# Optimization experiments

Measured on AMD Instinct MI355X. Metric: run time of the kernel, lower is better.

Reference implementation:

```python
import jax, jax.numpy as jnp
import numpy as np

V, E, H, O = 50000, 300, 1024, 5
B, T = 64, 512


def setup_inputs() -> dict:
    key = jax.random.key(0)
    ks = jax.random.split(key, 8)
    s_ih = 1.0 / np.sqrt(H)
    return {
        "x": jax.random.randint(ks[0], (B, T), 0, V, dtype=jnp.int32),
        "embeddings": jax.random.normal(ks[1], (V, E), dtype=jnp.float32),
        "W_ih": jax.random.uniform(ks[2], (3 * H, E), jnp.float32, -s_ih, s_ih),
        "W_hh": jax.random.uniform(ks[3], (3 * H, H), jnp.float32, -s_ih, s_ih),
        "b_ih": jax.random.uniform(ks[4], (3 * H,), jnp.float32, -s_ih, s_ih),
        "b_hh": jax.random.uniform(ks[5], (3 * H,), jnp.float32, -s_ih, s_ih),
        "W_fc": jax.random.uniform(ks[6], (O, H), jnp.float32, -s_ih, s_ih),
        "b_fc": jax.random.uniform(ks[7], (O,), jnp.float32, -s_ih, s_ih),
    }


def _gru_last_hidden(emb, W_ih, W_hh, b_ih, b_hh):
    # emb: [B, T, E] -> last hidden state [B, H]
    Hd = W_hh.shape[1]
    # Precompute input contributions for all timesteps: [B, T, 3H]
    gx_all = jnp.einsum("bte,ge->btg", emb, W_ih) + b_ih
    gx_all = jnp.swapaxes(gx_all, 0, 1)  # [T, B, 3H] for scan

    def step(h, gx):
        gh = h @ W_hh.T + b_hh  # [B, 3H]
        xr, xz, xn = jnp.split(gx, 3, axis=-1)
        hr, hz, hn = jnp.split(gh, 3, axis=-1)
        r = jax.nn.sigmoid(xr + hr)
        z = jax.nn.sigmoid(xz + hz)
        n = jnp.tanh(xn + r * hn)
        h_new = (1.0 - z) * n + z * h
        return h_new, None

    h0 = jnp.zeros((emb.shape[0], Hd), dtype=emb.dtype)
    h_last, _ = jax.lax.scan(step, h0, gx_all)
    return h_last


def reference(x, embeddings, W_ih, W_hh, b_ih, b_hh, W_fc, b_fc):
    emb = embeddings[x]  # [B, T, E] embedding lookup (frozen table)
    h_last = _gru_last_hidden(emb, W_ih, W_hh, b_ih, b_hh)  # [B, H]
    return h_last @ W_fc.T + b_fc  # [B, O]
```

## Files before the change

### kernel.cpp

```cpp
#include <hip/hip_runtime.h>
#include <hip/hip_bf16.h>

typedef unsigned short u16;
typedef unsigned int u32;
typedef unsigned long long u64;
typedef __attribute__((ext_vector_type(8))) short bf16x8;
typedef __attribute__((ext_vector_type(4))) float f32x4;
typedef __attribute__((ext_vector_type(4))) unsigned int u32x4;

#define MFMA16(a, b, c) __builtin_amdgcn_mfma_f32_16x16x32_bf16((a), (b), (c), 0, 0, 0)

static constexpr int Ee = 300, EP = 320, Hh = 1024, G3 = 3072;
static constexpr int Bb = 64, Tt = 512;

static constexpr long OFF_GX   = 0L;
static constexpr long OFF_EMB  = 201326592L;
static constexpr long OFF_WIH  = 222298112L;
static constexpr long OFF_WHH  = 224264192L;
static constexpr long OFF_HBUF = 230555648L;

__device__ __forceinline__ u16 f2bf(float f) {
    union { float f; unsigned u; } v; v.f = f;
    unsigned u = v.u;
    return (u16)((u + 0x7fffu + ((u >> 16) & 1u)) >> 16);
}
__device__ __forceinline__ float bf2f(u16 u) {
    union { unsigned u; float f; } v; v.u = ((unsigned)u) << 16;
    return v.f;
}
__device__ __forceinline__ float fast_sigmoid(float x) {
    return 1.f / (1.f + __expf(-x));
}
__device__ __forceinline__ float fast_tanh(float x) {
    float ax = fabsf(x);
    float e = __expf(-2.f * ax);
    float t = (1.f - e) / (1.f + e);
    return copysignf(t, x);
}

static constexpr long R0 = (long)Bb * Tt * EP;
static constexpr long R1 = (long)G3 * EP;
static constexpr long R2 = (long)G3 * Hh;
static constexpr long R3 = 131072;
static constexpr long R5 = 320;

__global__ void prep_kernel(const int* __restrict__ x, const float* __restrict__ emb,
                            const float* __restrict__ wih, const float* __restrict__ whh,
                            const float* __restrict__ bfc,
                            u16* __restrict__ emb_bf, u16* __restrict__ wih_bf,
                            u16* __restrict__ whh_bf, u32* __restrict__ h32,
                            float* __restrict__ out) {
    const long total = R0 + R1 + R2 + R3 + R5;
    for (long i = (long)blockIdx.x * blockDim.x + threadIdx.x; i < total;
         i += (long)gridDim.x * blockDim.x) {
        if (i < R0) {
            const int m = (int)(i / EP), k = (int)(i % EP);
            const int b = m & 63, t = m >> 6;
            u16 v = 0;
            if (k < Ee) {
                const int xi = x[b * Tt + t];
                v = f2bf(emb[(size_t)xi * Ee + k]);
            }
            emb_bf[i] = v;
        } else if (i < R0 + R1) {
            const long j = i - R0;
            const int k = (int)(j % EP);
            const int n = (int)(j / EP);
            wih_bf[j] = (k < Ee) ? f2bf(wih[(size_t)n * Ee + k]) : (u16)0;
        } else if (i < R0 + R1 + R2) {
            const long j = i - R0 - R1;
            whh_bf[j] = f2bf(whh[j]);
        } else if (i < R0 + R1 + R2 + R3) {
            const long j = i - R0 - R1 - R2;
            h32[j] = ((j >> 14) & 1) ? 0xFFFFu : 0u;
        } else {
            const long j = i - R0 - R1 - R2 - R3;
            out[j] = bfc[j % 5];
        }
    }
}

__global__ __launch_bounds__(256, 2)
void gx_gemm(const u16* __restrict__ A, const u16* __restrict__ Bm,
             const float* __restrict__ bih, u16* __restrict__ gx) {
    __shared__ __align__(16) u16 lA[128 * 32];
    __shared__ __align__(16) u16 lB[128 * 32];
    const int tid = threadIdx.x;
    const int lane = tid & 63;
    const int wv = tid >> 6;
    const int quad = lane >> 4, l15 = lane & 15;
    const int m0 = blockIdx.x * 128;
    const int n0 = blockIdx.y * 128;
    const int mo = (wv & 1) * 64, no = (wv >> 1) * 64;
    const int srow = tid >> 2;
    const int sseg = tid & 3;

    f32x4 acc[4][4] = {};

    for (int s = 0; s < 10; ++s) {
        const int k0 = s * 32;
        __syncthreads();
#pragma unroll
        for (int p = 0; p < 2; ++p) {
            const u16* ga = A + (size_t)(m0 + p * 64 + srow) * EP + k0 + sseg * 8;
            u16* la = &lA[p * 2048 + wv * 512];
            __builtin_amdgcn_global_load_lds(
                (const __attribute__((address_space(1))) void*)ga,
                (__attribute__((address_space(3))) void*)la, 16, 0, 0);
            const u16* gb = Bm + (size_t)(n0 + p * 64 + srow) * EP + k0 + sseg * 8;
            u16* lb = &lB[p * 2048 + wv * 512];
            __builtin_amdgcn_global_load_lds(
                (const __attribute__((address_space(1))) void*)gb,
                (__attribute__((address_space(3))) void*)lb, 16, 0, 0);
        }
        __syncthreads();

        bf16x8 af[4], bfr[4];
#pragma unroll
        for (int mt = 0; mt < 4; ++mt)
            af[mt] = *(const bf16x8*)&lA[(mo + mt * 16 + l15) * 32 + quad * 8];
#pragma unroll
        for (int nt = 0; nt < 4; ++nt)
            bfr[nt] = *(const bf16x8*)&lB[(no + nt * 16 + l15) * 32 + quad * 8];
#pragma unroll
        for (int mt = 0; mt < 4; ++mt)
#pragma unroll
            for (int nt = 0; nt < 4; ++nt)
                acc[mt][nt] = MFMA16(af[mt], bfr[nt], acc[mt][nt]);
    }

#pragma unroll
    for (int mt = 0; mt < 4; ++mt) {
        const int mg = m0 + mo + mt * 16 + quad * 4;
        const int t = mg >> 6, b0 = mg & 63;
#pragma unroll
        for (int nt = 0; nt < 4; ++nt) {
            const int n = n0 + no + nt * 16 + l15;
            const float bi = bih[n];
            ushort4 vv;
            vv.x = f2bf(acc[mt][nt][0] + bi);
            vv.y = f2bf(acc[mt][nt][1] + bi);
            vv.z = f2bf(acc[mt][nt][2] + bi);
            vv.w = f2bf(acc[mt][nt][3] + bi);
            *(ushort4*)&gx[((size_t)t * G3 + n) * 64 + b0] = vv;
        }
    }
}

__global__ __launch_bounds__(512, 2)
void scan_kernel(const u16* __restrict__ whh, const float* __restrict__ bhh,
                 const u16* __restrict__ gx, u32* __restrict__ hball,
                 const float* __restrict__ wfc, float* __restrict__ out) {
    __shared__ __align__(16) u16 lh[16 * 1032];
    __shared__ __align__(16) float red[2][3][4][16 * 20];

    const int bid = blockIdx.x;
    const int bg = bid >> 5;
    const int cg = bid & 31;
    const int tid = threadIdx.x;
    const int w = tid >> 6;
    const int lane = tid & 63;
    const int kq = w & 3;
    const int nh = w >> 2;
    const int quad = lane >> 4, l15 = lane & 15;
    const int c0 = cg * 32;
    const bool isGate = (w == 3) || (w == 4);
    const int gnh = (w == 3) ? 0 : 1;

    bf16x8 wf[3][8];
#pragma unroll
    for (int g = 0; g < 3; ++g) {
        const size_t rbase = (size_t)(g * 1024 + c0 + nh * 16 + l15) * 1024;
#pragma unroll
        for (int s = 0; s < 8; ++s)
            wf[g][s] = *(const bf16x8*)&whh[rbase + (kq * 8 + s) * 32 + quad * 8];
    }

    float bh[3][4];
    u16 gxv[3][4];
    float hO[4] = {0.f, 0.f, 0.f, 0.f};
    if (isGate) {
#pragma unroll
        for (int g = 0; g < 3; ++g)
#pragma unroll
            for (int jj = 0; jj < 4; ++jj) {
                const int jglob = c0 + gnh * 16 + quad * 4 + jj;
                bh[g][jj] = bhh[g * 1024 + jglob];
                gxv[g][jj] = gx[((size_t)g * 1024 + jglob) * 64 + bg * 16 + l15];
            }
    }

    u32* hb = hball + (size_t)bg * 32768;
    u64* lhq = (u64*)lh;
    const int t4 = tid << 2;
    const int srow0 = tid >> 8;
    const int sc4 = tid & 255;

    for (int t = 0; t < 512; ++t) {
        const u32* hs = hb + ((t & 1) << 14);
        const u32 tg = (u32)t;

        const u32* p0 = hs + t4;
        const u32* p1 = hs + 2048 + t4;
        const u32* p2 = hs + 4096 + t4;
        const u32* p3 = hs + 6144 + t4;
        const u32* p4 = hs + 8192 + t4;
        const u32* p5 = hs + 10240 + t4;
        const u32* p6 = hs + 12288 + t4;
        const u32* p7 = hs + 14336 + t4;
        u32x4 q0, q1, q2, q3, q4, q5, q6, q7;
        {
            u32 pend = 0xffu;
            do {
                if (pend & 0x01u) asm volatile("global_load_dwordx4 %0, %1, off sc0 sc1" : "=&v"(q0) : "v"(p0) : "memory");
                if (pend & 0x02u) asm volatile("global_load_dwordx4 %0, %1, off sc0 sc1" : "=&v"(q1) : "v"(p1) : "memory");
                if (pend & 0x04u) asm volatile("global_load_dwordx4 %0, %1, off sc0 sc1" : "=&v"(q2) : "v"(p2) : "memory");
                if (pend & 0x08u) asm volatile("global_load_dwordx4 %0, %1, off sc0 sc1" : "=&v"(q3) : "v"(p3) : "memory");
                if (pend & 0x10u) asm volatile("global_load_dwordx4 %0, %1, off sc0 sc1" : "=&v"(q4) : "v"(p4) : "memory");
                if (pend & 0x20u) asm volatile("global_load_dwordx4 %0, %1, off sc0 sc1" : "=&v"(q5) : "v"(p5) : "memory");
                if (pend & 0x40u) asm volatile("global_load_dwordx4 %0, %1, off sc0 sc1" : "=&v"(q6) : "v"(p6) : "memory");
                if (pend & 0x80u) asm volatile("global_load_dwordx4 %0, %1, off sc0 sc1" : "=&v"(q7) : "v"(p7) : "memory");
                asm volatile("s_waitcnt vmcnt(0)" ::: "memory");
                __builtin_amdgcn_sched_barrier(0);
                const u32 before = pend;
#define CHK(bit, qq)                                                          \
                if (pend & (bit)) {                                           \
                    const u32 d = ((qq.x ^ tg) | (qq.y ^ tg) |                \
                                   (qq.z ^ tg) | (qq.w ^ tg)) & 0xffffu;      \
                    if (__all(d == 0)) pend &= ~(u32)(bit);                   \
                }
                CHK(0x01u, q0) CHK(0x02u, q1) CHK(0x04u, q2) CHK(0x08u, q3)
                CHK(0x10u, q4) CHK(0x20u, q5) CHK(0x40u, q6) CHK(0x80u, q7)
#undef CHK
                if (pend && pend == before) __builtin_amdgcn_s_sleep(1);
            } while (pend);
        }

#define UNPK(rr, qq)                                                          \
        {                                                                     \
            const int row = (rr) * 2 + srow0;                                 \
            const u32 lo = (qq.x >> 16) | (qq.y & 0xffff0000u);               \
            const u32 hi = (qq.z >> 16) | (qq.w & 0xffff0000u);               \
            lhq[row * 258 + sc4] = (u64)lo | ((u64)hi << 32);                 \
        }
        UNPK(0, q0) UNPK(1, q1) UNPK(2, q2) UNPK(3, q3)
        UNPK(4, q4) UNPK(5, q5) UNPK(6, q6) UNPK(7, q7)
#undef UNPK
        __syncthreads();

        bf16x8 af[8];
#pragma unroll
        for (int s = 0; s < 8; ++s)
            af[s] = *(const bf16x8*)&lh[l15 * 1032 + kq * 256 + s * 32 + quad * 8];
        f32x4 acc[3] = {};
#pragma unroll
        for (int s = 0; s < 8; ++s) {
            acc[0] = MFMA16(af[s], wf[0][s], acc[0]);
            acc[1] = MFMA16(af[s], wf[1][s], acc[1]);
            acc[2] = MFMA16(af[s], wf[2][s], acc[2]);
        }
#pragma unroll
        for (int g = 0; g < 3; ++g)
#pragma unroll
            for (int r = 0; r < 4; ++r)
                red[nh][g][kq][(quad * 4 + r) * 20 + l15] = acc[g][r];
        __syncthreads();

        if (isGate) {
            f32x4 rr[3][4];
#pragma unroll
            for (int g = 0; g < 3; ++g)
#pragma unroll
                for (int k = 0; k < 4; ++k)
                    rr[g][k] = *(const f32x4*)&red[gnh][g][k][l15 * 20 + quad * 4];
            u32 wtag[4];
#pragma unroll
            for (int jj = 0; jj < 4; ++jj) {
                const float s0 = rr[0][0][jj] + rr[0][1][jj] + rr[0][2][jj] + rr[0][3][jj];
                const float s1 = rr[1][0][jj] + rr[1][1][jj] + rr[1][2][jj] + rr[1][3][jj];
                const float s2 = rr[2][0][jj] + rr[2][1][jj] + rr[2][2][jj] + rr[2][3][jj];
                const float rg = fast_sigmoid(bf2f(gxv[0][jj]) + s0 + bh[0][jj]);
                const float zg = fast_sigmoid(bf2f(gxv[1][jj]) + s1 + bh[1][jj]);
                const float ng = fast_tanh(bf2f(gxv[2][jj]) + rg * (s2 + bh[2][jj]));
                const float hv = (1.f - zg) * ng + zg * hO[jj];
                hO[jj] = hv;
                wtag[jj] = ((u32)f2bf(hv) << 16) | (u32)(t + 1);
            }
            if (t < 511) {
                u32* hn = hb + (((t + 1) & 1) << 14);
                const int widx = (l15 << 10) + c0 + gnh * 16 + (quad << 2);
                __hip_atomic_store((u64*)&hn[widx],
                                   (u64)wtag[0] | ((u64)wtag[1] << 32),
                                   __ATOMIC_RELAXED, __HIP_MEMORY_SCOPE_AGENT);
                __hip_atomic_store((u64*)&hn[widx + 2],
                                   (u64)wtag[2] | ((u64)wtag[3] << 32),
                                   __ATOMIC_RELAXED, __HIP_MEMORY_SCOPE_AGENT);
#pragma unroll
                for (int g = 0; g < 3; ++g)
#pragma unroll
                    for (int jj = 0; jj < 4; ++jj)
                        gxv[g][jj] = gx[((size_t)(t + 1) * G3 + g * 1024 + c0 +
                                         gnh * 16 + quad * 4 + jj) * 64 + bg * 16 + l15];
            }
        }
    }

    if (isGate) {
#pragma unroll
        for (int p = 0; p < 5; ++p) {
            float v = 0.f;
#pragma unroll
            for (int jj = 0; jj < 4; ++jj)
                v += hO[jj] * wfc[p * 1024 + c0 + gnh * 16 + quad * 4 + jj];
            v += __shfl_xor(v, 16);
            v += __shfl_xor(v, 32);
            if (quad == 0)
                atomicAdd(&out[(bg * 16 + l15) * 5 + p], v);
        }
    }
}

extern "C" void kernel_launch(void* const* d_in, const int* in_sizes, int n_in,
                              void* d_out, int out_size, void* d_ws, size_t ws_size,
                              hipStream_t stream) {
    const int*   x   = (const int*)d_in[0];
    const float* emb = (const float*)d_in[1];
    const float* wih = (const float*)d_in[2];
    const float* whh = (const float*)d_in[3];
    const float* bih = (const float*)d_in[4];
    const float* bhh = (const float*)d_in[5];
    const float* wfc = (const float*)d_in[6];
    const float* bfc = (const float*)d_in[7];
    float* out = (float*)d_out;

    char* ws = (char*)d_ws;
    u16*   gxw   = (u16*)(ws + OFF_GX);
    u16*   embbf = (u16*)(ws + OFF_EMB);
    u16*   wihbf = (u16*)(ws + OFF_WIH);
    u16*   whhbf = (u16*)(ws + OFF_WHH);
    u32*   h32   = (u32*)(ws + OFF_HBUF);

    prep_kernel<<<8192, 256, 0, stream>>>(x, emb, wih, whh, bfc, embbf, wihbf,
                                          whhbf, h32, out);

    gx_gemm<<<dim3(256, 24), 256, 0, stream>>>(embbf, wihbf, bih, gxw);

    scan_kernel<<<128, 512, 0, stream>>>(whhbf, bhh, gxw, h32, wfc, out);
}
```

Baseline: 2.302 ms.

## Poll hidden-state fragments directly per MFMA step, drop LDS staging and barrier

Each wave now spin-polls only the tagged hidden-state words it needs for each k-slice straight from global memory and feeds them into the MFMAs, instead of the whole block cooperatively loading all of h into LDS and then synchronizing. This removes one __syncthreads per timestep and the LDS round trip, and lets waves start MFMAs as soon as their own slice is ready. The reduction buffer is double-buffered by timestep parity so the remaining barrier is enough to keep steps apart. In exchange, each wave now issues redundant global loads of overlapping data and polls with many small waits. The launch bound hint is lowered to one block per CU.

Result: slower. 4.310 ms (+87.2%).

```diff
diff --git a/kernel.cpp b/kernel.cpp
--- a/kernel.cpp
+++ b/kernel.cpp
@@ -147,12 +147,11 @@
     }
 }
 
-__global__ __launch_bounds__(512, 2)
+__global__ __launch_bounds__(512, 1)
 void scan_kernel(const u16* __restrict__ whh, const float* __restrict__ bhh,
                  const u16* __restrict__ gx, u32* __restrict__ hball,
                  const float* __restrict__ wfc, float* __restrict__ out) {
-    __shared__ __align__(16) u16 lh[16 * 1032];
-    __shared__ __align__(16) float red[2][3][4][16 * 20];
+    __shared__ __align__(16) float red[2][2][3][4][16 * 20];
 
     const int bid = blockIdx.x;
     const int bg = bid >> 5;
@@ -191,79 +190,49 @@
     }
 
     u32* hb = hball + (size_t)bg * 32768;
-    u64* lhq = (u64*)lh;
-    const int t4 = tid << 2;
-    const int srow0 = tid >> 8;
-    const int sc4 = tid & 255;
+    const int wbase = l15 * 1024 + kq * 256 + quad * 8;
 
     for (int t = 0; t < 512; ++t) {
         const u32* hs = hb + ((t & 1) << 14);
         const u32 tg = (u32)t;
-
-        const u32* p0 = hs + t4;
-        const u32* p1 = hs + 2048 + t4;
-        const u32* p2 = hs + 4096 + t4;
-        const u32* p3 = hs + 6144 + t4;
-        const u32* p4 = hs + 8192 + t4;
-        const u32* p5 = hs + 10240 + t4;
-        const u32* p6 = hs + 12288 + t4;
-        const u32* p7 = hs + 14336 + t4;
-        u32x4 q0, q1, q2, q3, q4, q5, q6, q7;
-        {
-            u32 pend = 0xffu;
-            do {
-                if (pend & 0x01u) asm volatile("global_load_dwordx4 %0, %1, off sc0 sc1" : "=&v"(q0) : "v"(p0) : "memory");
-                if (pend & 0x02u) asm volatile("global_load_dwordx4 %0, %1, off sc0 sc1" : "=&v"(q1) : "v"(p1) : "memory");
-                if (pend & 0x04u) asm volatile("global_load_dwordx4 %0, %1, off sc0 sc1" : "=&v"(q2) : "v"(p2) : "memory");
-                if (pend & 0x08u) asm volatile("global_load_dwordx4 %0, %1, off sc0 sc1" : "=&v"(q3) : "v"(p3) : "memory");
-                if (pend & 0x10u) asm volatile("global_load_dwordx4 %0, %1, off sc0 sc1" : "=&v"(q4) : "v"(p4) : "memory");
-                if (pend & 0x20u) asm volatile("global_load_dwordx4 %0, %1, off sc0 sc1" : "=&v"(q5) : "v"(p5) : "memory");
-                if (pend & 0x40u) asm volatile("global_load_dwordx4 %0, %1, off sc0 sc1" : "=&v"(q6) : "v"(p6) : "memory");
-                if (pend & 0x80u) asm volatile("global_load_dwordx4 %0, %1, off sc0 sc1" : "=&v"(q7) : "v"(p7) : "memory");
-                asm volatile("s_waitcnt vmcnt(0)" ::: "memory");
+        const int par = t & 1;
+
+        f32x4 acc[3] = {};
+#pragma unroll
+        for (int s = 0; s < 8; ++s) {
+            const u32* p0 = hs + wbase + s * 32;
+            const u32* p1 = p0 + 4;
+            u32x4 a0, a1;
+            for (;;) {
+                asm volatile(
+                    "global_load_dwordx4 %0, %2, off sc0 sc1\n\t"
+                    "global_load_dwordx4 %1, %3, off sc0 sc1\n\t"
+                    "s_waitcnt vmcnt(0)"
+                    : "=&v"(a0), "=&v"(a1)
+                    : "v"(p0), "v"(p1)
+                    : "memory");
                 __builtin_amdgcn_sched_barrier(0);
-                const u32 before = pend;
-#define CHK(bit, qq)                                                          \
-                if (pend & (bit)) {                                           \
-                    const u32 d = ((qq.x ^ tg) | (qq.y ^ tg) |                \
-                                   (qq.z ^ tg) | (qq.w ^ tg)) & 0xffffu;      \
-                    if (__all(d == 0)) pend &= ~(u32)(bit);                   \
-                }
-                CHK(0x01u, q0) CHK(0x02u, q1) CHK(0x04u, q2) CHK(0x08u, q3)
-                CHK(0x10u, q4) CHK(0x20u, q5) CHK(0x40u, q6) CHK(0x80u, q7)
-#undef CHK
-                if (pend && pend == before) __builtin_amdgcn_s_sleep(1);
-            } while (pend);
-        }
-
-#define UNPK(rr, qq)                                                          \
-        {                                                                     \
-            const int row = (rr) * 2 + srow0;                                 \
-            const u32 lo = (qq.x >> 16) | (qq.y & 0xffff0000u);               \
-            const u32 hi = (qq.z >> 16) | (qq.w & 0xffff0000u);               \
-            lhq[row * 258 + sc4] = (u64)lo | ((u64)hi << 32);                 \
-        }
-        UNPK(0, q0) UNPK(1, q1) UNPK(2, q2) UNPK(3, q3)
-        UNPK(4, q4) UNPK(5, q5) UNPK(6, q6) UNPK(7, q7)
-#undef UNPK
-        __syncthreads();
-
-        bf16x8 af[8];
-#pragma unroll
-        for (int s = 0; s < 8; ++s)
-            af[s] = *(const bf16x8*)&lh[l15 * 1032 + kq * 256 + s * 32 + quad * 8];
-        f32x4 acc[3] = {};
-#pragma unroll
-        for (int s = 0; s < 8; ++s) {
-            acc[0] = MFMA16(af[s], wf[0][s], acc[0]);
-            acc[1] = MFMA16(af[s], wf[1][s], acc[1]);
-            acc[2] = MFMA16(af[s], wf[2][s], acc[2]);
-        }
+                const u32 d = ((a0.x ^ tg) | (a0.y ^ tg) | (a0.z ^ tg) | (a0.w ^ tg) |
+                               (a1.x ^ tg) | (a1.y ^ tg) | (a1.z ^ tg) | (a1.w ^ tg)) &
+                              0xffffu;
+                if (__all(d == 0)) break;
+                __builtin_amdgcn_s_sleep(1);
+            }
+            union { u32 u[4]; bf16x8 v; } fr;
+            fr.u[0] = (a0.x >> 16) | (a0.y & 0xffff0000u);
+            fr.u[1] = (a0.z >> 16) | (a0.w & 0xffff0000u);
+            fr.u[2] = (a1.x >> 16) | (a1.y & 0xffff0000u);
+            fr.u[3] = (a1.z >> 16) | (a1.w & 0xffff0000u);
+            acc[0] = MFMA16(fr.v, wf[0][s], acc[0]);
+            acc[1] = MFMA16(fr.v, wf[1][s], acc[1]);
+            acc[2] = MFMA16(fr.v, wf[2][s], acc[2]);
+        }
+
 #pragma unroll
         for (int g = 0; g < 3; ++g)
 #pragma unroll
             for (int r = 0; r < 4; ++r)
-                red[nh][g][kq][(quad * 4 + r) * 20 + l15] = acc[g][r];
+                red[par][nh][g][kq][(quad * 4 + r) * 20 + l15] = acc[g][r];
         __syncthreads();
 
         if (isGate) {
@@ -272,7 +241,7 @@
             for (int g = 0; g < 3; ++g)
 #pragma unroll
                 for (int k = 0; k < 4; ++k)
-                    rr[g][k] = *(const f32x4*)&red[gnh][g][k][l15 * 20 + quad * 4];
+                    rr[g][k] = *(const f32x4*)&red[par][gnh][g][k][l15 * 20 + quad * 4];
             u32 wtag[4];
 #pragma unroll
             for (int jj = 0; jj < 4; ++jj) {
```

## Add per-block progress flags and prefetch next-step gx in GRU scan

Applied to the files above, without the earlier changes.

Before pulling the hidden state, the persistent scan kernel now polls per-producer progress flags, one per 64-byte-padded slot, instead of spinning on the whole 16KB tagged h buffer. It then loads h once and checks the tags, retrying only when needed. The gx values for the next timestep are prefetched with inline asm ushort loads and overlapped with the h loads, using a double-buffered register set and an unroll by two. __syncthreads is swapped for an lgkmcnt wait plus s_barrier. This adds a flag store per step and spin polling on flags, and relies on relaxed ordering between the h stores and the flag store, so the tag check remains the correctness fallback.

New measurement: 2.423 ms. +5.3%, slower.

```diff
diff --git a/kernel.cpp b/kernel.cpp
--- a/kernel.cpp
+++ b/kernel.cpp
@@ -18,6 +18,7 @@
 static constexpr long OFF_WIH  = 222298112L;
 static constexpr long OFF_WHH  = 224264192L;
 static constexpr long OFF_HBUF = 230555648L;
+static constexpr long OFF_FLAG = 231079936L;
 
 __device__ __forceinline__ u16 f2bf(float f) {
     union { float f; unsigned u; } v; v.f = f;
@@ -38,10 +39,17 @@
     return copysignf(t, x);
 }
 
+#define BAR_LDS()                                             \
+    do {                                                      \
+        asm volatile("s_waitcnt lgkmcnt(0)" ::: "memory");    \
+        __builtin_amdgcn_s_barrier();                         \
+    } while (0)
+
 static constexpr long R0 = (long)Bb * Tt * EP;
 static constexpr long R1 = (long)G3 * EP;
 static constexpr long R2 = (long)G3 * Hh;
 static constexpr long R3 = 131072;
+static constexpr long R4 = 4096;
 static constexpr long R5 = 320;
 
 __global__ void prep_kernel(const int* __restrict__ x, const float* __restrict__ emb,
@@ -49,8 +57,8 @@
                             const float* __restrict__ bfc,
                             u16* __restrict__ emb_bf, u16* __restrict__ wih_bf,
                             u16* __restrict__ whh_bf, u32* __restrict__ h32,
-                            float* __restrict__ out) {
-    const long total = R0 + R1 + R2 + R3 + R5;
+                            int* __restrict__ flags, float* __restrict__ out) {
+    const long total = R0 + R1 + R2 + R3 + R4 + R5;
     for (long i = (long)blockIdx.x * blockDim.x + threadIdx.x; i < total;
          i += (long)gridDim.x * blockDim.x) {
         if (i < R0) {
@@ -73,8 +81,10 @@
         } else if (i < R0 + R1 + R2 + R3) {
             const long j = i - R0 - R1 - R2;
             h32[j] = ((j >> 14) & 1) ? 0xFFFFu : 0u;
+        } else if (i < R0 + R1 + R2 + R3 + R4) {
+            flags[i - R0 - R1 - R2 - R3] = 0;
         } else {
-            const long j = i - R0 - R1 - R2 - R3;
+            const long j = i - R0 - R1 - R2 - R3 - R4;
             out[j] = bfc[j % 5];
         }
     }
@@ -150,7 +160,8 @@
 __global__ __launch_bounds__(512, 2)
 void scan_kernel(const u16* __restrict__ whh, const float* __restrict__ bhh,
                  const u16* __restrict__ gx, u32* __restrict__ hball,
-                 const float* __restrict__ wfc, float* __restrict__ out) {
+                 const float* __restrict__ wfc, float* __restrict__ out,
+                 int* __restrict__ flags) {
     __shared__ __align__(16) u16 lh[16 * 1032];
     __shared__ __align__(16) float red[2][3][4][16 * 20];
 
@@ -166,6 +177,7 @@
     const int c0 = cg * 32;
     const bool isGate = (w == 3) || (w == 4);
     const int gnh = (w == 3) ? 0 : 1;
+    const int jbase = c0 + gnh * 16 + quad * 4;
 
     bf16x8 wf[3][8];
 #pragma unroll
@@ -177,28 +189,51 @@
     }
 
     float bh[3][4];
-    u16 gxv[3][4];
+    u32 gxA[12], gxB[12];
     float hO[4] = {0.f, 0.f, 0.f, 0.f};
     if (isGate) {
 #pragma unroll
         for (int g = 0; g < 3; ++g)
 #pragma unroll
             for (int jj = 0; jj < 4; ++jj) {
-                const int jglob = c0 + gnh * 16 + quad * 4 + jj;
-                bh[g][jj] = bhh[g * 1024 + jglob];
-                gxv[g][jj] = gx[((size_t)g * 1024 + jglob) * 64 + bg * 16 + l15];
-            }
-    }
+                bh[g][jj] = bhh[g * 1024 + jbase + jj];
+                gxA[g * 4 + jj] =
+                    (u32)gx[((size_t)(g * 1024 + jbase + jj)) * 64 + bg * 16 + l15];
+            }
+    }
+    const long GSTEP = (long)G3 * 64 * 2;
+    const char* gp0 = (const char*)gx +
+                      (((size_t)1 * G3 + 0 * 1024 + jbase) * 64 + bg * 16 + l15) * 2;
+    const char* gp1 = gp0 + (size_t)1024 * 64 * 2;
+    const char* gp2 = gp1 + (size_t)1024 * 64 * 2;
 
     u32* hb = hball + (size_t)bg * 32768;
-    u64* lhq = (u64*)lh;
+    int* gflag = &flags[(bg * 64 + lane) * 16];
+    int* myflag = &flags[(bg * 64 + cg * 2 + gnh) * 16];
     const int t4 = tid << 2;
     const int srow0 = tid >> 8;
     const int sc4 = tid & 255;
-
-    for (int t = 0; t < 512; ++t) {
+    u64* lhq = (u64*)lh;
+
+    auto body = [&](const int t, u32 (&gxCur)[12], u32 (&gxNxt)[12]) {
         const u32* hs = hb + ((t & 1) << 14);
         const u32 tg = (u32)t;
+
+        int v = __hip_atomic_load(gflag, __ATOMIC_RELAXED, __HIP_MEMORY_SCOPE_AGENT);
+        bool done = (v >= t);
+        while (!__all(done)) {
+            __builtin_amdgcn_s_sleep(1);
+            if (!done) {
+                v = __hip_atomic_load(gflag, __ATOMIC_RELAXED, __HIP_MEMORY_SCOPE_AGENT);
+                done = (v >= t);
+            }
+        }
+        if (isGate)
+            asm volatile("" : "+v"(gxCur[0]), "+v"(gxCur[1]), "+v"(gxCur[2]),
+                              "+v"(gxCur[3]), "+v"(gxCur[4]), "+v"(gxCur[5]),
+                              "+v"(gxCur[6]), "+v"(gxCur[7]), "+v"(gxCur[8]),
+                              "+v"(gxCur[9]), "+v"(gxCur[10]), "+v"(gxCur[11])
+                            : "v"(v));
 
         const u32* p0 = hs + t4;
         const u32* p1 = hs + 2048 + t4;
@@ -209,32 +244,83 @@
         const u32* p6 = hs + 12288 + t4;
         const u32* p7 = hs + 14336 + t4;
         u32x4 q0, q1, q2, q3, q4, q5, q6, q7;
-        {
-            u32 pend = 0xffu;
-            do {
-                if (pend & 0x01u) asm volatile("global_load_dwordx4 %0, %1, off sc0 sc1" : "=&v"(q0) : "v"(p0) : "memory");
-                if (pend & 0x02u) asm volatile("global_load_dwordx4 %0, %1, off sc0 sc1" : "=&v"(q1) : "v"(p1) : "memory");
-                if (pend & 0x04u) asm volatile("global_load_dwordx4 %0, %1, off sc0 sc1" : "=&v"(q2) : "v"(p2) : "memory");
-                if (pend & 0x08u) asm volatile("global_load_dwordx4 %0, %1, off sc0 sc1" : "=&v"(q3) : "v"(p3) : "memory");
-                if (pend & 0x10u) asm volatile("global_load_dwordx4 %0, %1, off sc0 sc1" : "=&v"(q4) : "v"(p4) : "memory");
-                if (pend & 0x20u) asm volatile("global_load_dwordx4 %0, %1, off sc0 sc1" : "=&v"(q5) : "v"(p5) : "memory");
-                if (pend & 0x40u) asm volatile("global_load_dwordx4 %0, %1, off sc0 sc1" : "=&v"(q6) : "v"(p6) : "memory");
-                if (pend & 0x80u) asm volatile("global_load_dwordx4 %0, %1, off sc0 sc1" : "=&v"(q7) : "v"(p7) : "memory");
-                asm volatile("s_waitcnt vmcnt(0)" ::: "memory");
-                __builtin_amdgcn_sched_barrier(0);
-                const u32 before = pend;
-#define CHK(bit, qq)                                                          \
-                if (pend & (bit)) {                                           \
-                    const u32 d = ((qq.x ^ tg) | (qq.y ^ tg) |                \
-                                   (qq.z ^ tg) | (qq.w ^ tg)) & 0xffffu;      \
-                    if (__all(d == 0)) pend &= ~(u32)(bit);                   \
-                }
-                CHK(0x01u, q0) CHK(0x02u, q1) CHK(0x04u, q2) CHK(0x08u, q3)
-                CHK(0x10u, q4) CHK(0x20u, q5) CHK(0x40u, q6) CHK(0x80u, q7)
-#undef CHK
-                if (pend && pend == before) __builtin_amdgcn_s_sleep(1);
-            } while (pend);
-        }
+        asm volatile(
+            "global_load_dwordx4 %0, %8, off sc0 sc1\n\t"
+            "global_load_dwordx4 %1, %9, off sc0 sc1\n\t"
+            "global_load_dwordx4 %2, %10, off sc0 sc1\n\t"
+            "global_load_dwordx4 %3, %11, off sc0 sc1\n\t"
+            "global_load_dwordx4 %4, %12, off sc0 sc1\n\t"
+            "global_load_dwordx4 %5, %13, off sc0 sc1\n\t"
+            "global_load_dwordx4 %6, %14, off sc0 sc1\n\t"
+            "global_load_dwordx4 %7, %15, off sc0 sc1"
+            : "=&v"(q0), "=&v"(q1), "=&v"(q2), "=&v"(q3),
+              "=&v"(q4), "=&v"(q5), "=&v"(q6), "=&v"(q7)
+            : "v"(p0), "v"(p1), "v"(p2), "v"(p3),
+              "v"(p4), "v"(p5), "v"(p6), "v"(p7)
+            : "memory");
+        if (isGate && t < 511) {
+            asm volatile(
+                "global_load_ushort %0, %4, off\n\t"
+                "global_load_ushort %1, %4, off offset:128\n\t"
+                "global_load_ushort %2, %4, off offset:256\n\t"
+                "global_load_ushort %3, %4, off offset:384"
+                : "=&v"(gxNxt[0]), "=&v"(gxNxt[1]), "=&v"(gxNxt[2]), "=&v"(gxNxt[3])
+                : "v"(gp0) : "memory");
+            asm volatile(
+                "global_load_ushort %0, %4, off\n\t"
+                "global_load_ushort %1, %4, off offset:128\n\t"
+                "global_load_ushort %2, %4, off offset:256\n\t"
+                "global_load_ushort %3, %4, off offset:384"
+                : "=&v"(gxNxt[4]), "=&v"(gxNxt[5]), "=&v"(gxNxt[6]), "=&v"(gxNxt[7])
+                : "v"(gp1) : "memory");
+            asm volatile(
+                "global_load_ushort %0, %4, off\n\t"
+                "global_load_ushort %1, %4, off offset:128\n\t"
+                "global_load_ushort %2, %4, off offset:256\n\t"
+                "global_load_ushort %3, %4, off offset:384"
+                : "=&v"(gxNxt[8]), "=&v"(gxNxt[9]), "=&v"(gxNxt[10]), "=&v"(gxNxt[11])
+                : "v"(gp2) : "memory");
+            asm volatile("s_waitcnt vmcnt(12)" ::: "memory");
+        } else {
+            asm volatile("s_waitcnt vmcnt(0)" ::: "memory");
+        }
+        gp0 += GSTEP; gp1 += GSTEP; gp2 += GSTEP;
+        __builtin_amdgcn_sched_barrier(0);
+
+        u32 pend = 0;
+#define TCHK(bit, qq)                                                         \
+        {                                                                     \
+            const u32 d = ((qq.x ^ tg) | (qq.y ^ tg) |                        \
+                           (qq.z ^ tg) | (qq.w ^ tg)) & 0xffffu;              \
+            if (!__all(d == 0)) pend |= (bit);                                \
+        }
+        TCHK(0x01u, q0) TCHK(0x02u, q1) TCHK(0x04u, q2) TCHK(0x08u, q3)
+        TCHK(0x10u, q4) TCHK(0x20u, q5) TCHK(0x40u, q6) TCHK(0x80u, q7)
+        while (pend) {
+            __builtin_amdgcn_s_sleep(1);
+            if (pend & 0x01u) asm volatile("global_load_dwordx4 %0, %1, off sc0 sc1" : "=&v"(q0) : "v"(p0) : "memory");
+            if (pend & 0x02u) asm volatile("global_load_dwordx4 %0, %1, off sc0 sc1" : "=&v"(q1) : "v"(p1) : "memory");
+            if (pend & 0x04u) asm volatile("global_load_dwordx4 %0, %1, off sc0 sc1" : "=&v"(q2) : "v"(p2) : "memory");
+            if (pend & 0x08u) asm volatile("global_load_dwordx4 %0, %1, off sc0 sc1" : "=&v"(q3) : "v"(p3) : "memory");
+            if (pend & 0x10u) asm volatile("global_load_dwordx4 %0, %1, off sc0 sc1" : "=&v"(q4) : "v"(p4) : "memory");
+            if (pend & 0x20u) asm volatile("global_load_dwordx4 %0, %1, off sc0 sc1" : "=&v"(q5) : "v"(p5) : "memory");
+            if (pend & 0x40u) asm volatile("global_load_dwordx4 %0, %1, off sc0 sc1" : "=&v"(q6) : "v"(p6) : "memory");
+            if (pend & 0x80u) asm volatile("global_load_dwordx4 %0, %1, off sc0 sc1" : "=&v"(q7) : "v"(p7) : "memory");
+            asm volatile("s_waitcnt vmcnt(0)" ::: "memory");
+            __builtin_amdgcn_sched_barrier(0);
+            u32 np = 0;
+#define RCHK(bit, qq)                                                         \
+            if (pend & (bit)) {                                               \
+                const u32 d = ((qq.x ^ tg) | (qq.y ^ tg) |                    \
+                               (qq.z ^ tg) | (qq.w ^ tg)) & 0xffffu;          \
+                if (!__all(d == 0)) np |= (bit);                              \
+            }
+            RCHK(0x01u, q0) RCHK(0x02u, q1) RCHK(0x04u, q2) RCHK(0x08u, q3)
+            RCHK(0x10u, q4) RCHK(0x20u, q5) RCHK(0x40u, q6) RCHK(0x80u, q7)
+#undef RCHK
+            pend = np;
+        }
+#undef TCHK
 
 #define UNPK(rr, qq)                                                          \
         {                                                                     \
@@ -246,7 +332,7 @@
         UNPK(0, q0) UNPK(1, q1) UNPK(2, q2) UNPK(3, q3)
         UNPK(4, q4) UNPK(5, q5) UNPK(6, q6) UNPK(7, q7)
 #undef UNPK
-        __syncthreads();
+        BAR_LDS();
 
         bf16x8 af[8];
 #pragma unroll
@@ -264,7 +350,7 @@
 #pragma unroll
             for (int r = 0; r < 4; ++r)
                 red[nh][g][kq][(quad * 4 + r) * 20 + l15] = acc[g][r];
-        __syncthreads();
+        BAR_LDS();
 
         if (isGate) {
             f32x4 rr[3][4];
@@ -279,30 +365,32 @@
                 const float s0 = rr[0][0][jj] + rr[0][1][jj] + rr[0][2][jj] + rr[0][3][jj];
                 const float s1 = rr[1][0][jj] + rr[1][1][jj] + rr[1][2][jj] + rr[1][3][jj];
                 const float s2 = rr[2][0][jj] + rr[2][1][jj] + rr[2][2][jj] + rr[2][3][jj];
-                const float rg = fast_sigmoid(bf2f(gxv[0][jj]) + s0 + bh[0][jj]);
-                const float zg = fast_sigmoid(bf2f(gxv[1][jj]) + s1 + bh[1][jj]);
-                const float ng = fast_tanh(bf2f(gxv[2][jj]) + rg * (s2 + bh[2][jj]));
+                const float rg = fast_sigmoid(bf2f((u16)gxCur[0 * 4 + jj]) + s0 + bh[0][jj]);
+                const float zg = fast_sigmoid(bf2f((u16)gxCur[1 * 4 + jj]) + s1 + bh[1][jj]);
+                const float ng = fast_tanh(bf2f((u16)gxCur[2 * 4 + jj]) + rg * (s2 + bh[2][jj]));
                 const float hv = (1.f - zg) * ng + zg * hO[jj];
                 hO[jj] = hv;
                 wtag[jj] = ((u32)f2bf(hv) << 16) | (u32)(t + 1);
             }
             if (t < 511) {
                 u32* hn = hb + (((t + 1) & 1) << 14);
-                const int widx = (l15 << 10) + c0 + gnh * 16 + (quad << 2);
-                __hip_atomic_store((u64*)&hn[widx],
-                                   (u64)wtag[0] | ((u64)wtag[1] << 32),
-                                   __ATOMIC_RELAXED, __HIP_MEMORY_SCOPE_AGENT);
-                __hip_atomic_store((u64*)&hn[widx + 2],
-                                   (u64)wtag[2] | ((u64)wtag[3] << 32),
-                                   __ATOMIC_RELAXED, __HIP_MEMORY_SCOPE_AGENT);
-#pragma unroll
-                for (int g = 0; g < 3; ++g)
-#pragma unroll
-                    for (int jj = 0; jj < 4; ++jj)
-                        gxv[g][jj] = gx[((size_t)(t + 1) * G3 + g * 1024 + c0 +
-                                         gnh * 16 + quad * 4 + jj) * 64 + bg * 16 + l15];
-            }
-        }
+                const int widx = (l15 << 10) + jbase;
+                const u64 d0 = (u64)wtag[0] | ((u64)wtag[1] << 32);
+                const u64 d1 = (u64)wtag[2] | ((u64)wtag[3] << 32);
+                asm volatile("global_store_dwordx2 %0, %1, off sc0 sc1"
+                             :: "v"((u64*)&hn[widx]), "v"(d0) : "memory");
+                asm volatile("global_store_dwordx2 %0, %1, off sc0 sc1"
+                             :: "v"((u64*)&hn[widx + 2]), "v"(d1) : "memory");
+                if (lane == 0)
+                    __hip_atomic_store(myflag, t + 1, __ATOMIC_RELAXED,
+                                       __HIP_MEMORY_SCOPE_AGENT);
+            }
+        }
+    };
+
+    for (int t = 0; t < 512; t += 2) {
+        body(t, gxA, gxB);
+        body(t + 1, gxB, gxA);
     }
 
     if (isGate) {
@@ -311,7 +399,7 @@
             float v = 0.f;
 #pragma unroll
             for (int jj = 0; jj < 4; ++jj)
-                v += hO[jj] * wfc[p * 1024 + c0 + gnh * 16 + quad * 4 + jj];
+                v += hO[jj] * wfc[p * 1024 + jbase + jj];
             v += __shfl_xor(v, 16);
             v += __shfl_xor(v, 32);
             if (quad == 0)
@@ -339,11 +427,12 @@
     u16*   wihbf = (u16*)(ws + OFF_WIH);
     u16*   whhbf = (u16*)(ws + OFF_WHH);
     u32*   h32   = (u32*)(ws + OFF_HBUF);
+    int*   flags = (int*)(ws + OFF_FLAG);
 
     prep_kernel<<<8192, 256, 0, stream>>>(x, emb, wih, whh, bfc, embbf, wihbf,
-                                          whhbf, h32, out);
+                                          whhbf, h32, flags, out);
 
     gx_gemm<<<dim3(256, 24), 256, 0, stream>>>(embbf, wihbf, bih, gxw);
 
-    scan_kernel<<<128, 512, 0, stream>>>(whhbf, bhh, gxw, h32, wfc, out);
-}
+    scan_kernel<<<128, 512, 0, stream>>>(whhbf, bhh, gxw, h32, wfc, out, flags);
+}
```
